# Performance work log

Hardware: AMD Instinct MI355X
Metric: run time of the kernel (lower is better)

## Reference

```python
import jax, jax.numpy as jnp
import numpy as np

T, H, E, K, I = 4096, 1024, 8, 2, 2048
EPS = 1e-5


def setup_inputs() -> dict:
    key = jax.random.key(0)
    ks = jax.random.split(key, 5)
    xavier = jax.nn.initializers.variance_scaling(1.0, 'fan_avg', 'uniform', dtype=jnp.float32)
    return {
        'x': jax.random.normal(ks[0], (T, H), dtype=jnp.float32),
        'scale': jnp.ones((H,), dtype=jnp.float32),
        'gate_kernel': xavier(ks[1], (H, E), jnp.float32),
        'gate_bias': jnp.zeros((E,), dtype=jnp.float32),
        'mlp1_weight': xavier(ks[2], (E, 2 * I, H), jnp.float32),
        'mlp1_bias': jnp.zeros((E, 2 * I), dtype=jnp.float32),
        'mlp2_weight': xavier(ks[3], (E, H, I), jnp.float32),
        'mlp2_bias': jnp.zeros((E, H), dtype=jnp.float32),
    }


def reference(x, scale, gate_kernel, gate_bias, mlp1_weight, mlp1_bias, mlp2_weight, mlp2_bias):
    # RMSNorm in fp32
    t = x.astype(jnp.float32)
    rms = jnp.sqrt(jnp.mean(t * t, axis=-1, keepdims=True) + EPS)
    normed = ((t / rms) * scale).astype(x.dtype)  # [T, H]

    # Gating: top-k experts + softmax over selected logits
    gate_logits = normed @ gate_kernel + gate_bias  # [T, E]
    expert_logits, expert_indices = jax.lax.top_k(gate_logits, K)  # [T, K]
    expert_weights = jax.nn.softmax(expert_logits, axis=-1)  # [T, K]

    # Dense all-expert SwiGLU MLP (faithful to vmap-over-experts original)
    # mlp1_weight: [E, 2I, H] -> mlp1: [E, T, 2I]
    mlp1 = jnp.einsum('td,efd->etf', normed, mlp1_weight) + mlp1_bias[:, None, :]
    gate_part = jnp.minimum(mlp1[..., :I], 7.0)
    linear_part = jnp.clip(mlp1[..., I:], -7.0, 7.0)
    swish_gate = gate_part * jax.nn.sigmoid(1.702 * gate_part)
    activated = swish_gate * (linear_part + 1.0)  # [E, T, I]
    # mlp2_weight: [E, H, I] -> expert_outputs: [T, E, H]
    expert_outputs = (jnp.einsum('eti,ehi->eth', activated, mlp2_weight)
                      + mlp2_bias[:, None, :]).transpose(1, 0, 2)

    # Scatter top-k weights to dense [T, E] and combine
    one_hot = jax.nn.one_hot(expert_indices, E, dtype=expert_outputs.dtype)  # [T, K, E]
    dense_gate_weights = jnp.sum(one_hot * expert_weights[..., None], axis=1)  # [T, E]
    fused = jnp.einsum('teh,te->th', expert_outputs, dense_gate_weights)
    return x + fused
```

## Files before the change

### kernel.cpp

```cpp
#include <hip/hip_runtime.h>
#include <hip/hip_bf16.h>
#include <math.h>

#define T_ 4096
#define H_ 1024
#define E_ 8
#define I_ 2048
#define EPS_ 1e-5f

using bf16x8 = __attribute__((ext_vector_type(8))) short;
using f32x4  = __attribute__((ext_vector_type(4))) float;

static __device__ __forceinline__ unsigned short f2bf(float f) {
    union { float f; unsigned int u; } v; v.f = f;
    unsigned int u = v.u;
    u += 0x7fffu + ((u >> 16) & 1u);
    return (unsigned short)(u >> 16);
}

static __device__ __forceinline__ void gld16(const unsigned short* g, unsigned short* l) {
    __builtin_amdgcn_global_load_lds(
        (const __attribute__((address_space(1))) unsigned int*)g,
        (__attribute__((address_space(3))) unsigned int*)l,
        16, 0, 0);
}

__global__ __launch_bounds__(256) void k_convert(
    const float* __restrict__ src, unsigned short* __restrict__ dst)
{
    size_t i = (size_t)blockIdx.x * 256 + threadIdx.x;
    const float4* s = (const float4*)src + i * 2;
    float4 a = s[0], b = s[1];
    ushort4 lo, hi;
    lo.x = f2bf(a.x); lo.y = f2bf(a.y); lo.z = f2bf(a.z); lo.w = f2bf(a.w);
    hi.x = f2bf(b.x); hi.y = f2bf(b.y); hi.z = f2bf(b.z); hi.w = f2bf(b.w);
    ((ushort4*)dst)[i * 2]     = lo;
    ((ushort4*)dst)[i * 2 + 1] = hi;
}

__global__ __launch_bounds__(256) void k_norm_gate(
    const float* __restrict__ x, const float* __restrict__ scale,
    const float* __restrict__ gk, const float* __restrict__ gb,
    unsigned short* __restrict__ normed_bf,
    int* __restrict__ counts, int* __restrict__ tok_list, float* __restrict__ wtok)
{
    int tid = threadIdx.x;
    int wave = tid >> 6, lane = tid & 63;
    int t = blockIdx.x * 4 + wave;
    const float* xr = x + (size_t)t * H_;
    int h0 = lane * 16;

    float4 xv[4], sv[4];
    #pragma unroll
    for (int c = 0; c < 4; c++) {
        xv[c] = *(const float4*)(xr + h0 + c * 4);
        sv[c] = *(const float4*)(scale + h0 + c * 4);
    }
    float ss = 0.f;
    #pragma unroll
    for (int c = 0; c < 4; c++)
        ss += xv[c].x*xv[c].x + xv[c].y*xv[c].y + xv[c].z*xv[c].z + xv[c].w*xv[c].w;
    #pragma unroll
    for (int off = 32; off; off >>= 1) ss += __shfl_xor(ss, off);
    float inv = 1.0f / sqrtf(ss / (float)H_ + EPS_);

    float nv[16];
    #pragma unroll
    for (int c = 0; c < 4; c++) {
        nv[c*4+0] = xv[c].x * inv * sv[c].x;
        nv[c*4+1] = xv[c].y * inv * sv[c].y;
        nv[c*4+2] = xv[c].z * inv * sv[c].z;
        nv[c*4+3] = xv[c].w * inv * sv[c].w;
    }
    #pragma unroll
    for (int c = 0; c < 4; c++) {
        ushort4 nb;
        nb.x = f2bf(nv[c*4+0]); nb.y = f2bf(nv[c*4+1]);
        nb.z = f2bf(nv[c*4+2]); nb.w = f2bf(nv[c*4+3]);
        *(ushort4*)(normed_bf + (size_t)t * H_ + h0 + c * 4) = nb;
    }

    float p[E_];
    #pragma unroll
    for (int e = 0; e < E_; e++) p[e] = 0.f;
    #pragma unroll
    for (int j = 0; j < 16; j++) {
        const float4* g4 = (const float4*)(gk + (size_t)(h0 + j) * E_);
        float4 a = g4[0], b = g4[1];
        float n = nv[j];
        p[0] += n*a.x; p[1] += n*a.y; p[2] += n*a.z; p[3] += n*a.w;
        p[4] += n*b.x; p[5] += n*b.y; p[6] += n*b.z; p[7] += n*b.w;
    }
    #pragma unroll
    for (int e = 0; e < E_; e++) {
        #pragma unroll
        for (int off = 32; off; off >>= 1) p[e] += __shfl_xor(p[e], off);
    }
    if (lane == 0) {
        int b0 = -1, b1 = -1; float l0 = -1e30f, l1 = -1e30f;
        #pragma unroll
        for (int e = 0; e < E_; e++) {
            float lg = p[e] + gb[e];
            if (lg > l0) { l1 = l0; b1 = b0; l0 = lg; b0 = e; }
            else if (lg > l1) { l1 = lg; b1 = e; }
        }
        float e1 = expf(l1 - l0);
        float w0 = 1.f / (1.f + e1);
        float w1 = e1 / (1.f + e1);
        wtok[t * 2 + 0] = w0;
        wtok[t * 2 + 1] = w1;
        int p0 = atomicAdd(&counts[b0], 1);
        tok_list[b0 * T_ + p0] = t * 2 + 0;
        int p1 = atomicAdd(&counts[b1], 1);
        tok_list[b1 * T_ + p1] = t * 2 + 1;
    }
}

__global__ __launch_bounds__(256) void k_mlp1(
    const unsigned short* __restrict__ w1b,
    const float* __restrict__ b1,
    const unsigned short* __restrict__ normed_bf,
    const int* __restrict__ counts, const int* __restrict__ tok_list,
    unsigned short* __restrict__ act)
{
    int e = blockIdx.z;
    int Ne = counts[e];
    int mt0 = blockIdx.y * 128;
    if (mt0 >= Ne) return;
    int it0 = blockIdx.x * 64;
    int tid = threadIdx.x;
    int lane = tid & 63, w = tid >> 6;
    int quad = lane >> 4, m16 = lane & 15;
    int wr = w >> 1, wc = w & 1;

    __shared__ unsigned short lA[128 * 64];
    __shared__ unsigned short lBg[64 * 64];
    __shared__ unsigned short lBl[64 * 64];
    __shared__ int ls_tk[128];

    if (tid < 128) {
        int slot = mt0 + tid;
        ls_tk[tid] = (slot < Ne) ? tok_list[e * T_ + slot] : -1;
    }

    int lr = lane >> 3;
    int pc = lane & 7;

    const unsigned short* srcA[4];
    #pragma unroll
    for (int it = 0; it < 4; it++) {
        int r = w * 32 + it * 8 + lr;
        int slot = mt0 + r;
        int tk = (slot < Ne) ? tok_list[e * T_ + slot] : 0;
        srcA[it] = normed_bf + (size_t)(tk >> 1) * H_ + ((pc ^ (r & 7)) << 3);
    }
    const size_t w1base = (size_t)e * 2 * I_ * H_;
    const unsigned short* srcG[2];
    const unsigned short* srcL[2];
    #pragma unroll
    for (int it = 0; it < 2; it++) {
        int r = w * 16 + it * 8 + lr;
        srcG[it] = w1b + w1base + (size_t)(it0 + r) * H_ + ((pc ^ (r & 7)) << 3);
        srcL[it] = srcG[it] + (size_t)I_ * H_;
    }

    f32x4 accg[4][2], accl[4][2];
    #pragma unroll
    for (int mi = 0; mi < 4; mi++)
        #pragma unroll
        for (int ni = 0; ni < 2; ni++) {
            accg[mi][ni] = (f32x4){0.f, 0.f, 0.f, 0.f};
            accl[mi][ni] = (f32x4){0.f, 0.f, 0.f, 0.f};
        }

    for (int kk = 0; kk < H_; kk += 64) {
        __syncthreads();
        #pragma unroll
        for (int it = 0; it < 4; it++)
            gld16(srcA[it] + kk, &lA[(w * 32 + it * 8) * 64]);
        #pragma unroll
        for (int it = 0; it < 2; it++) {
            gld16(srcG[it] + kk, &lBg[(w * 16 + it * 8) * 64]);
            gld16(srcL[it] + kk, &lBl[(w * 16 + it * 8) * 64]);
        }
        __syncthreads();
        int m7 = m16 & 7;
        #pragma unroll
        for (int ks = 0; ks < 2; ks++) {
            int jj = ks * 4 + quad;
            bf16x8 af[4], bg[2], bl[2];
            #pragma unroll
            for (int mi = 0; mi < 4; mi++)
                af[mi] = *(const bf16x8*)(&lA[(wr * 64 + mi * 16 + m16) * 64 + ((jj ^ m7) << 3)]);
            #pragma unroll
            for (int ni = 0; ni < 2; ni++) {
                bg[ni] = *(const bf16x8*)(&lBg[(wc * 32 + ni * 16 + m16) * 64 + ((jj ^ m7) << 3)]);
                bl[ni] = *(const bf16x8*)(&lBl[(wc * 32 + ni * 16 + m16) * 64 + ((jj ^ m7) << 3)]);
            }
            #pragma unroll
            for (int mi = 0; mi < 4; mi++)
                #pragma unroll
                for (int ni = 0; ni < 2; ni++) {
                    accg[mi][ni] = __builtin_amdgcn_mfma_f32_16x16x32_bf16(
                        af[mi], bg[ni], accg[mi][ni], 0, 0, 0);
                    accl[mi][ni] = __builtin_amdgcn_mfma_f32_16x16x32_bf16(
                        af[mi], bl[ni], accl[mi][ni], 0, 0, 0);
                }
        }
    }

    const float* b1g = b1 + (size_t)e * 2 * I_;
    const float* b1l = b1g + I_;
    #pragma unroll
    for (int mi = 0; mi < 4; mi++) {
        #pragma unroll
        for (int reg = 0; reg < 4; reg++) {
            int row = wr * 64 + mi * 16 + quad * 4 + reg;
            int tk = ls_tk[row];
            if (tk < 0) continue;
            #pragma unroll
            for (int ni = 0; ni < 2; ni++) {
                int i = it0 + wc * 32 + ni * 16 + m16;
                float g = accg[mi][ni][reg] + b1g[i];
                float l = accl[mi][ni][reg] + b1l[i];
                g = fminf(g, 7.f);
                l = fminf(fmaxf(l, -7.f), 7.f);
                float sw = g / (1.f + expf(-1.702f * g));
                act[(size_t)tk * I_ + i] = f2bf(sw * (l + 1.f));
            }
        }
    }
}

__global__ __launch_bounds__(256) void k_mlp2(
    const unsigned short* __restrict__ w2b,
    const float* __restrict__ b2,
    const unsigned short* __restrict__ act,
    const int* __restrict__ counts, const int* __restrict__ tok_list,
    float* __restrict__ ybuf)
{
    int e = blockIdx.z;
    int Ne = counts[e];
    int mt0 = blockIdx.y * 128;
    if (mt0 >= Ne) return;
    int ht0 = blockIdx.x * 128;
    int tid = threadIdx.x;
    int lane = tid & 63, w = tid >> 6;
    int quad = lane >> 4, m16 = lane & 15;
    int wr = w >> 1, wc = w & 1;

    __shared__ unsigned short lA[128 * 64];
    __shared__ unsigned short lB[128 * 64];
    __shared__ int ls_tk[128];

    if (tid < 128) {
        int slot = mt0 + tid;
        ls_tk[tid] = (slot < Ne) ? tok_list[e * T_ + slot] : -1;
    }

    int lr = lane >> 3;
    int pc = lane & 7;

    const unsigned short* srcA[4];
    #pragma unroll
    for (int it = 0; it < 4; it++) {
        int r = w * 32 + it * 8 + lr;
        int slot = mt0 + r;
        int tk = (slot < Ne) ? tok_list[e * T_ + slot] : 0;
        srcA[it] = act + (size_t)tk * I_ + ((pc ^ (r & 7)) << 3);
    }
    const size_t w2base = (size_t)e * H_ * I_;
    const unsigned short* srcB[4];
    #pragma unroll
    for (int it = 0; it < 4; it++) {
        int r = w * 32 + it * 8 + lr;
        srcB[it] = w2b + w2base + (size_t)(ht0 + r) * I_ + ((pc ^ (r & 7)) << 3);
    }

    f32x4 acc[4][4];
    #pragma unroll
    for (int mi = 0; mi < 4; mi++)
        #pragma unroll
        for (int ni = 0; ni < 4; ni++)
            acc[mi][ni] = (f32x4){0.f, 0.f, 0.f, 0.f};

    for (int kk = 0; kk < I_; kk += 64) {
        __syncthreads();
        #pragma unroll
        for (int it = 0; it < 4; it++)
            gld16(srcA[it] + kk, &lA[(w * 32 + it * 8) * 64]);
        #pragma unroll
        for (int it = 0; it < 4; it++)
            gld16(srcB[it] + kk, &lB[(w * 32 + it * 8) * 64]);
        __syncthreads();
        int m7 = m16 & 7;
        #pragma unroll
        for (int ks = 0; ks < 2; ks++) {
            int jj = ks * 4 + quad;
            bf16x8 af[4], bv[4];
            #pragma unroll
            for (int mi = 0; mi < 4; mi++)
                af[mi] = *(const bf16x8*)(&lA[(wr * 64 + mi * 16 + m16) * 64 + ((jj ^ m7) << 3)]);
            #pragma unroll
            for (int ni = 0; ni < 4; ni++)
                bv[ni] = *(const bf16x8*)(&lB[(wc * 64 + ni * 16 + m16) * 64 + ((jj ^ m7) << 3)]);
            #pragma unroll
            for (int mi = 0; mi < 4; mi++)
                #pragma unroll
                for (int ni = 0; ni < 4; ni++)
                    acc[mi][ni] = __builtin_amdgcn_mfma_f32_16x16x32_bf16(
                        af[mi], bv[ni], acc[mi][ni], 0, 0, 0);
        }
    }

    const float* b2e = b2 + (size_t)e * H_;
    #pragma unroll
    for (int mi = 0; mi < 4; mi++) {
        #pragma unroll
        for (int reg = 0; reg < 4; reg++) {
            int row = wr * 64 + mi * 16 + quad * 4 + reg;
            int tk = ls_tk[row];
            if (tk < 0) continue;
            #pragma unroll
            for (int ni = 0; ni < 4; ni++) {
                int h = ht0 + wc * 64 + ni * 16 + m16;
                ybuf[(size_t)tk * H_ + h] = acc[mi][ni][reg] + b2e[h];
            }
        }
    }
}

__global__ __launch_bounds__(256) void k_combine(
    const float* __restrict__ x, const float* __restrict__ ybuf,
    const float* __restrict__ wtok, float* __restrict__ out)
{
    int t = blockIdx.x;
    int tid = threadIdx.x;
    float w0 = wtok[t * 2 + 0];
    float w1 = wtok[t * 2 + 1];
    float4 xv = ((const float4*)(x + (size_t)t * H_))[tid];
    float4 y0 = ((const float4*)(ybuf + (size_t)(t * 2) * H_))[tid];
    float4 y1 = ((const float4*)(ybuf + (size_t)(t * 2 + 1) * H_))[tid];
    float4 o;
    o.x = xv.x + w0 * y0.x + w1 * y1.x;
    o.y = xv.y + w0 * y0.y + w1 * y1.y;
    o.z = xv.z + w0 * y0.z + w1 * y1.z;
    o.w = xv.w + w0 * y0.w + w1 * y1.w;
    ((float4*)(out + (size_t)t * H_))[tid] = o;
}

extern "C" void kernel_launch(void* const* d_in, const int* in_sizes, int n_in,
                              void* d_out, int out_size, void* d_ws, size_t ws_size,
                              hipStream_t stream) {
    const float* x     = (const float*)d_in[0];
    const float* scale = (const float*)d_in[1];
    const float* gk    = (const float*)d_in[2];
    const float* gb    = (const float*)d_in[3];
    const float* w1    = (const float*)d_in[4];
    const float* b1    = (const float*)d_in[5];
    const float* w2    = (const float*)d_in[6];
    const float* b2    = (const float*)d_in[7];
    float* out = (float*)d_out;

    char* ws = (char*)d_ws;
    const size_t MB = 1024 * 1024;
    unsigned short* normed_bf = (unsigned short*)ws;
    unsigned short* act       = (unsigned short*)(ws + 8 * MB);
    unsigned short* w1b       = (unsigned short*)(ws + 40 * MB);
    float*          ybuf      = (float*)(ws + 40 * MB);
    unsigned short* w2b       = (unsigned short*)(ws + 104 * MB);
    char* ctl                 = ws + 136 * MB;
    int*   counts   = (int*)ctl;
    int*   tok_list = (int*)(ctl + 256);
    float* wtok     = (float*)(ctl + 256 + (size_t)E_ * T_ * 4);

    hipMemsetAsync(counts, 0, E_ * sizeof(int), stream);

    k_norm_gate<<<dim3(T_ / 4), dim3(256), 0, stream>>>(
        x, scale, gk, gb, normed_bf, counts, tok_list, wtok);
    k_convert<<<dim3((E_ * 2 * I_ * H_) / (256 * 8)), dim3(256), 0, stream>>>(w1, w1b);
    k_convert<<<dim3((E_ * H_ * I_) / (256 * 8)), dim3(256), 0, stream>>>(w2, w2b);

    k_mlp1<<<dim3(I_ / 64, T_ / 128, E_), dim3(256), 0, stream>>>(
        w1b, b1, normed_bf, counts, tok_list, act);
    k_mlp2<<<dim3(H_ / 128, T_ / 128, E_), dim3(256), 0, stream>>>(
        w2b, b2, act, counts, tok_list, ybuf);
    k_combine<<<dim3(T_), dim3(256), 0, stream>>>(x, ybuf, wtok, out);
}
```

Measured before the change: 589.8 us.

## Double-buffer LDS tiles in both expert GEMM kernels to overlap loads with MFMA

Both the MLP1 and MLP2 grouped-GEMM kernels now keep two LDS buffers. The global-to-LDS load for the next K slice is issued before the MFMA work on the current slice, and the loop runs two slices per iteration. The aim is to hide global memory latency behind compute and drop one barrier per slice. In exchange, LDS use per block doubles (about 64KB in both kernels), which may lower occupancy. There is also a subtle risk: the asynchronous LDS writes are only ordered by the barriers, so correctness relies on the barrier waiting for outstanding vmcnt.

```diff
diff --git a/kernel.cpp b/kernel.cpp
--- a/kernel.cpp
+++ b/kernel.cpp
@@ -133,9 +133,9 @@
     int quad = lane >> 4, m16 = lane & 15;
     int wr = w >> 1, wc = w & 1;
 
-    __shared__ unsigned short lA[128 * 64];
-    __shared__ unsigned short lBg[64 * 64];
-    __shared__ unsigned short lBl[64 * 64];
+    __shared__ unsigned short lA[2][128 * 64];
+    __shared__ unsigned short lBg[2][64 * 64];
+    __shared__ unsigned short lBl[2][64 * 64];
     __shared__ int ls_tk[128];
 
     if (tid < 128) {
@@ -173,41 +173,58 @@
             accl[mi][ni] = (f32x4){0.f, 0.f, 0.f, 0.f};
         }
 
-    for (int kk = 0; kk < H_; kk += 64) {
+    int m7 = m16 & 7;
+
+#define STAGE1(buf, kk)                                                       \
+    {                                                                          \
+        _Pragma("unroll")                                                      \
+        for (int it = 0; it < 4; it++)                                         \
+            gld16(srcA[it] + (kk), &lA[buf][(w * 32 + it * 8) * 64]);          \
+        _Pragma("unroll")                                                      \
+        for (int it = 0; it < 2; it++) {                                       \
+            gld16(srcG[it] + (kk), &lBg[buf][(w * 16 + it * 8) * 64]);         \
+            gld16(srcL[it] + (kk), &lBl[buf][(w * 16 + it * 8) * 64]);         \
+        }                                                                      \
+    }
+
+#define COMP1(buf)                                                             \
+    {                                                                          \
+        _Pragma("unroll")                                                      \
+        for (int ks = 0; ks < 2; ks++) {                                       \
+            int jj = ks * 4 + quad;                                            \
+            bf16x8 af[4], bg[2], bl[2];                                        \
+            _Pragma("unroll")                                                  \
+            for (int mi = 0; mi < 4; mi++)                                     \
+                af[mi] = *(const bf16x8*)(&lA[buf][(wr * 64 + mi * 16 + m16) * 64 + ((jj ^ m7) << 3)]); \
+            _Pragma("unroll")                                                  \
+            for (int ni = 0; ni < 2; ni++) {                                   \
+                bg[ni] = *(const bf16x8*)(&lBg[buf][(wc * 32 + ni * 16 + m16) * 64 + ((jj ^ m7) << 3)]); \
+                bl[ni] = *(const bf16x8*)(&lBl[buf][(wc * 32 + ni * 16 + m16) * 64 + ((jj ^ m7) << 3)]); \
+            }                                                                  \
+            _Pragma("unroll")                                                  \
+            for (int mi = 0; mi < 4; mi++)                                     \
+                _Pragma("unroll")                                              \
+                for (int ni = 0; ni < 2; ni++) {                               \
+                    accg[mi][ni] = __builtin_amdgcn_mfma_f32_16x16x32_bf16(    \
+                        af[mi], bg[ni], accg[mi][ni], 0, 0, 0);                \
+                    accl[mi][ni] = __builtin_amdgcn_mfma_f32_16x16x32_bf16(    \
+                        af[mi], bl[ni], accl[mi][ni], 0, 0, 0);                \
+                }                                                              \
+        }                                                                      \
+    }
+
+    STAGE1(0, 0);
+    __syncthreads();
+    for (int kk = 0; kk < H_; kk += 128) {
+        STAGE1(1, kk + 64);
+        COMP1(0);
         __syncthreads();
-        #pragma unroll
-        for (int it = 0; it < 4; it++)
-            gld16(srcA[it] + kk, &lA[(w * 32 + it * 8) * 64]);
-        #pragma unroll
-        for (int it = 0; it < 2; it++) {
-            gld16(srcG[it] + kk, &lBg[(w * 16 + it * 8) * 64]);
-            gld16(srcL[it] + kk, &lBl[(w * 16 + it * 8) * 64]);
-        }
+        if (kk + 128 < H_) STAGE1(0, kk + 128);
+        COMP1(1);
         __syncthreads();
-        int m7 = m16 & 7;
-        #pragma unroll
-        for (int ks = 0; ks < 2; ks++) {
-            int jj = ks * 4 + quad;
-            bf16x8 af[4], bg[2], bl[2];
-            #pragma unroll
-            for (int mi = 0; mi < 4; mi++)
-                af[mi] = *(const bf16x8*)(&lA[(wr * 64 + mi * 16 + m16) * 64 + ((jj ^ m7) << 3)]);
-            #pragma unroll
-            for (int ni = 0; ni < 2; ni++) {
-                bg[ni] = *(const bf16x8*)(&lBg[(wc * 32 + ni * 16 + m16) * 64 + ((jj ^ m7) << 3)]);
-                bl[ni] = *(const bf16x8*)(&lBl[(wc * 32 + ni * 16 + m16) * 64 + ((jj ^ m7) << 3)]);
-            }
-            #pragma unroll
-            for (int mi = 0; mi < 4; mi++)
-                #pragma unroll
-                for (int ni = 0; ni < 2; ni++) {
-                    accg[mi][ni] = __builtin_amdgcn_mfma_f32_16x16x32_bf16(
-                        af[mi], bg[ni], accg[mi][ni], 0, 0, 0);
-                    accl[mi][ni] = __builtin_amdgcn_mfma_f32_16x16x32_bf16(
-                        af[mi], bl[ni], accl[mi][ni], 0, 0, 0);
-                }
-        }
-    }
+    }
+#undef STAGE1
+#undef COMP1
 
     const float* b1g = b1 + (size_t)e * 2 * I_;
     const float* b1l = b1g + I_;
@@ -249,8 +266,8 @@
     int quad = lane >> 4, m16 = lane & 15;
     int wr = w >> 1, wc = w & 1;
 
-    __shared__ unsigned short lA[128 * 64];
-    __shared__ unsigned short lB[128 * 64];
+    __shared__ unsigned short lA[2][128 * 64];
+    __shared__ unsigned short lB[2][128 * 64];
     __shared__ int ls_tk[128];
 
     if (tid < 128) {
@@ -284,34 +301,51 @@
         for (int ni = 0; ni < 4; ni++)
             acc[mi][ni] = (f32x4){0.f, 0.f, 0.f, 0.f};
 
-    for (int kk = 0; kk < I_; kk += 64) {
+    int m7 = m16 & 7;
+
+#define STAGE2(buf, kk)                                                       \
+    {                                                                          \
+        _Pragma("unroll")                                                      \
+        for (int it = 0; it < 4; it++)                                         \
+            gld16(srcA[it] + (kk), &lA[buf][(w * 32 + it * 8) * 64]);          \
+        _Pragma("unroll")                                                      \
+        for (int it = 0; it < 4; it++)                                         \
+            gld16(srcB[it] + (kk), &lB[buf][(w * 32 + it * 8) * 64]);          \
+    }
+
+#define COMP2(buf)                                                             \
+    {                                                                          \
+        _Pragma("unroll")                                                      \
+        for (int ks = 0; ks < 2; ks++) {                                       \
+            int jj = ks * 4 + quad;                                            \
+            bf16x8 af[4], bv[4];                                               \
+            _Pragma("unroll")                                                  \
+            for (int mi = 0; mi < 4; mi++)                                     \
+                af[mi] = *(const bf16x8*)(&lA[buf][(wr * 64 + mi * 16 + m16) * 64 + ((jj ^ m7) << 3)]); \
+            _Pragma("unroll")                                                  \
+            for (int ni = 0; ni < 4; ni++)                                     \
+                bv[ni] = *(const bf16x8*)(&lB[buf][(wc * 64 + ni * 16 + m16) * 64 + ((jj ^ m7) << 3)]); \
+            _Pragma("unroll")                                                  \
+            for (int mi = 0; mi < 4; mi++)                                     \
+                _Pragma("unroll")                                              \
+                for (int ni = 0; ni < 4; ni++)                                 \
+                    acc[mi][ni] = __builtin_amdgcn_mfma_f32_16x16x32_bf16(     \
+                        af[mi], bv[ni], acc[mi][ni], 0, 0, 0);                 \
+        }                                                                      \
+    }
+
+    STAGE2(0, 0);
+    __syncthreads();
+    for (int kk = 0; kk < I_; kk += 128) {
+        STAGE2(1, kk + 64);
+        COMP2(0);
         __syncthreads();
-        #pragma unroll
-        for (int it = 0; it < 4; it++)
-            gld16(srcA[it] + kk, &lA[(w * 32 + it * 8) * 64]);
-        #pragma unroll
-        for (int it = 0; it < 4; it++)
-            gld16(srcB[it] + kk, &lB[(w * 32 + it * 8) * 64]);
+        if (kk + 128 < I_) STAGE2(0, kk + 128);
+        COMP2(1);
         __syncthreads();
-        int m7 = m16 & 7;
-        #pragma unroll
-        for (int ks = 0; ks < 2; ks++) {
-            int jj = ks * 4 + quad;
-            bf16x8 af[4], bv[4];
-            #pragma unroll
-            for (int mi = 0; mi < 4; mi++)
-                af[mi] = *(const bf16x8*)(&lA[(wr * 64 + mi * 16 + m16) * 64 + ((jj ^ m7) << 3)]);
-            #pragma unroll
-            for (int ni = 0; ni < 4; ni++)
-                bv[ni] = *(const bf16x8*)(&lB[(wc * 64 + ni * 16 + m16) * 64 + ((jj ^ m7) << 3)]);
-            #pragma unroll
-            for (int mi = 0; mi < 4; mi++)
-                #pragma unroll
-                for (int ni = 0; ni < 4; ni++)
-                    acc[mi][ni] = __builtin_amdgcn_mfma_f32_16x16x32_bf16(
-                        af[mi], bv[ni], acc[mi][ni], 0, 0, 0);
-        }
-    }
+    }
+#undef STAGE2
+#undef COMP2
 
     const float* b2e = b2 + (size_t)e * H_;
     #pragma unroll
```

After: 609.1 us. 3.3% more time.

## Register-prefetch GEMM tiles, retile mlp1, and merge weight conversion kernels

Applied to the files above, without the earlier changes.

Both expert GEMM kernels stop using direct global-to-LDS loads. They now prefetch the next K-slice into registers while computing the current one, then write it into swizzled LDS, so global latency overlaps with MFMA work. mlp1 is retiled from 128 tokens by 64 I-columns to 64 tokens by 128 I-columns, which reuses each token row across more weight columns. The two fp32-to-bf16 weight conversions are merged into one launch. In exchange the kernels use more registers and write to LDS through VGPRs, and the smaller token tile reads the mlp1 weights more often.

```diff
diff --git a/kernel.cpp b/kernel.cpp
--- a/kernel.cpp
+++ b/kernel.cpp
@@ -18,17 +18,17 @@
     return (unsigned short)(u >> 16);
 }
 
-static __device__ __forceinline__ void gld16(const unsigned short* g, unsigned short* l) {
-    __builtin_amdgcn_global_load_lds(
-        (const __attribute__((address_space(1))) unsigned int*)g,
-        (__attribute__((address_space(3))) unsigned int*)l,
-        16, 0, 0);
-}
-
-__global__ __launch_bounds__(256) void k_convert(
-    const float* __restrict__ src, unsigned short* __restrict__ dst)
-{
-    size_t i = (size_t)blockIdx.x * 256 + threadIdx.x;
+__global__ __launch_bounds__(256) void k_convert2(
+    const float* __restrict__ s1, unsigned short* __restrict__ d1,
+    const float* __restrict__ s2, unsigned short* __restrict__ d2,
+    int nb1)
+{
+    int bx = blockIdx.x;
+    const float* src;
+    unsigned short* dst;
+    size_t i;
+    if (bx < nb1) { src = s1; dst = d1; i = (size_t)bx * 256 + threadIdx.x; }
+    else          { src = s2; dst = d2; i = (size_t)(bx - nb1) * 256 + threadIdx.x; }
     const float4* s = (const float4*)src + i * 2;
     float4 a = s[0], b = s[1];
     ushort4 lo, hi;
@@ -125,82 +125,87 @@
 {
     int e = blockIdx.z;
     int Ne = counts[e];
-    int mt0 = blockIdx.y * 128;
+    int mt0 = blockIdx.y * 64;
     if (mt0 >= Ne) return;
-    int it0 = blockIdx.x * 64;
+    int it0 = blockIdx.x * 128;
     int tid = threadIdx.x;
     int lane = tid & 63, w = tid >> 6;
     int quad = lane >> 4, m16 = lane & 15;
     int wr = w >> 1, wc = w & 1;
-
-    __shared__ unsigned short lA[128 * 64];
-    __shared__ unsigned short lBg[64 * 64];
-    __shared__ unsigned short lBl[64 * 64];
-    __shared__ int ls_tk[128];
-
-    if (tid < 128) {
-        int slot = mt0 + tid;
-        ls_tk[tid] = (slot < Ne) ? tok_list[e * T_ + slot] : -1;
-    }
-
-    int lr = lane >> 3;
-    int pc = lane & 7;
-
-    const unsigned short* srcA[4];
-    #pragma unroll
-    for (int it = 0; it < 4; it++) {
-        int r = w * 32 + it * 8 + lr;
-        int slot = mt0 + r;
-        int tk = (slot < Ne) ? tok_list[e * T_ + slot] : 0;
-        srcA[it] = normed_bf + (size_t)(tk >> 1) * H_ + ((pc ^ (r & 7)) << 3);
-    }
-    const size_t w1base = (size_t)e * 2 * I_ * H_;
-    const unsigned short* srcG[2];
-    const unsigned short* srcL[2];
-    #pragma unroll
-    for (int it = 0; it < 2; it++) {
-        int r = w * 16 + it * 8 + lr;
-        srcG[it] = w1b + w1base + (size_t)(it0 + r) * H_ + ((pc ^ (r & 7)) << 3);
-        srcL[it] = srcG[it] + (size_t)I_ * H_;
-    }
-
-    f32x4 accg[4][2], accl[4][2];
-    #pragma unroll
-    for (int mi = 0; mi < 4; mi++)
-        #pragma unroll
-        for (int ni = 0; ni < 2; ni++) {
+    int m7 = m16 & 7;
+
+    __shared__ unsigned short lA[64 * 64];
+    __shared__ unsigned short lBg[128 * 64];
+    __shared__ unsigned short lBl[128 * 64];
+
+    f32x4 accg[2][4], accl[2][4];
+    #pragma unroll
+    for (int mi = 0; mi < 2; mi++)
+        #pragma unroll
+        for (int ni = 0; ni < 4; ni++) {
             accg[mi][ni] = (f32x4){0.f, 0.f, 0.f, 0.f};
             accl[mi][ni] = (f32x4){0.f, 0.f, 0.f, 0.f};
         }
 
+    const size_t w1base = (size_t)e * 2 * I_ * H_;
+    int rA = tid >> 3, sgA = tid & 7;
+    int jA = sgA ^ (rA & 7);
+    int rB = tid >> 1, sgB = tid & 1;
+
+    int slot0 = mt0 + rA, slot1 = mt0 + rA + 32;
+    int tk0 = (slot0 < Ne) ? tok_list[e * T_ + slot0] : -1;
+    int tk1 = (slot1 < Ne) ? tok_list[e * T_ + slot1] : -1;
+    const unsigned short* sA0 = normed_bf + (size_t)((tk0 < 0) ? 0 : (tk0 >> 1)) * H_ + sgA * 8;
+    const unsigned short* sA1 = normed_bf + (size_t)((tk1 < 0) ? 0 : (tk1 >> 1)) * H_ + sgA * 8;
+    const unsigned short* sG = w1b + w1base + (size_t)(it0 + rB) * H_ + sgB * 32;
+    const unsigned short* sL = sG + (size_t)I_ * H_;
+
+    uint4 ra0, ra1, rg[4], rl[4];
+    ra0 = *(const uint4*)(sA0);
+    ra1 = *(const uint4*)(sA1);
+    #pragma unroll
+    for (int q = 0; q < 4; q++) {
+        rg[q] = ((const uint4*)sG)[q];
+        rl[q] = ((const uint4*)sL)[q];
+    }
+
     for (int kk = 0; kk < H_; kk += 64) {
         __syncthreads();
-        #pragma unroll
-        for (int it = 0; it < 4; it++)
-            gld16(srcA[it] + kk, &lA[(w * 32 + it * 8) * 64]);
-        #pragma unroll
-        for (int it = 0; it < 2; it++) {
-            gld16(srcG[it] + kk, &lBg[(w * 16 + it * 8) * 64]);
-            gld16(srcL[it] + kk, &lBl[(w * 16 + it * 8) * 64]);
+        *(uint4*)(&lA[rA * 64 + jA * 8])        = ra0;
+        *(uint4*)(&lA[(rA + 32) * 64 + jA * 8]) = ra1;
+        #pragma unroll
+        for (int q = 0; q < 4; q++) {
+            int jc = (4 * sgB + q) ^ (rB & 7);
+            *(uint4*)(&lBg[rB * 64 + jc * 8]) = rg[q];
+            *(uint4*)(&lBl[rB * 64 + jc * 8]) = rl[q];
         }
         __syncthreads();
-        int m7 = m16 & 7;
-        #pragma unroll
-        for (int ks = 0; ks < 2; ks++) {
-            int jj = ks * 4 + quad;
-            bf16x8 af[4], bg[2], bl[2];
-            #pragma unroll
-            for (int mi = 0; mi < 4; mi++)
-                af[mi] = *(const bf16x8*)(&lA[(wr * 64 + mi * 16 + m16) * 64 + ((jj ^ m7) << 3)]);
-            #pragma unroll
-            for (int ni = 0; ni < 2; ni++) {
-                bg[ni] = *(const bf16x8*)(&lBg[(wc * 32 + ni * 16 + m16) * 64 + ((jj ^ m7) << 3)]);
-                bl[ni] = *(const bf16x8*)(&lBl[(wc * 32 + ni * 16 + m16) * 64 + ((jj ^ m7) << 3)]);
-            }
-            #pragma unroll
-            for (int mi = 0; mi < 4; mi++)
+        if (kk + 64 < H_) {
+            int k2 = kk + 64;
+            ra0 = *(const uint4*)(sA0 + k2);
+            ra1 = *(const uint4*)(sA1 + k2);
+            #pragma unroll
+            for (int q = 0; q < 4; q++) {
+                rg[q] = ((const uint4*)(sG + k2))[q];
+                rl[q] = ((const uint4*)(sL + k2))[q];
+            }
+        }
+        #pragma unroll
+        for (int ks2 = 0; ks2 < 2; ks2++) {
+            int jj = ks2 * 4 + quad;
+            bf16x8 af[2], bg[4], bl[4];
+            #pragma unroll
+            for (int mi = 0; mi < 2; mi++)
+                af[mi] = *(const bf16x8*)(&lA[(wr * 32 + mi * 16 + m16) * 64 + ((jj ^ m7) << 3)]);
+            #pragma unroll
+            for (int ni = 0; ni < 4; ni++) {
+                bg[ni] = *(const bf16x8*)(&lBg[(wc * 64 + ni * 16 + m16) * 64 + ((jj ^ m7) << 3)]);
+                bl[ni] = *(const bf16x8*)(&lBl[(wc * 64 + ni * 16 + m16) * 64 + ((jj ^ m7) << 3)]);
+            }
+            #pragma unroll
+            for (int mi = 0; mi < 2; mi++)
                 #pragma unroll
-                for (int ni = 0; ni < 2; ni++) {
+                for (int ni = 0; ni < 4; ni++) {
                     accg[mi][ni] = __builtin_amdgcn_mfma_f32_16x16x32_bf16(
                         af[mi], bg[ni], accg[mi][ni], 0, 0, 0);
                     accl[mi][ni] = __builtin_amdgcn_mfma_f32_16x16x32_bf16(
@@ -212,15 +217,16 @@
     const float* b1g = b1 + (size_t)e * 2 * I_;
     const float* b1l = b1g + I_;
     #pragma unroll
-    for (int mi = 0; mi < 4; mi++) {
+    for (int mi = 0; mi < 2; mi++) {
         #pragma unroll
         for (int reg = 0; reg < 4; reg++) {
-            int row = wr * 64 + mi * 16 + quad * 4 + reg;
-            int tk = ls_tk[row];
-            if (tk < 0) continue;
-            #pragma unroll
-            for (int ni = 0; ni < 2; ni++) {
-                int i = it0 + wc * 32 + ni * 16 + m16;
+            int row = wr * 32 + mi * 16 + quad * 4 + reg;
+            int slot = mt0 + row;
+            if (slot >= Ne) continue;
+            int tk = tok_list[e * T_ + slot];
+            #pragma unroll
+            for (int ni = 0; ni < 4; ni++) {
+                int i = it0 + wc * 64 + ni * 16 + m16;
                 float g = accg[mi][ni][reg] + b1g[i];
                 float l = accl[mi][ni][reg] + b1l[i];
                 g = fminf(g, 7.f);
@@ -248,34 +254,10 @@
     int lane = tid & 63, w = tid >> 6;
     int quad = lane >> 4, m16 = lane & 15;
     int wr = w >> 1, wc = w & 1;
+    int m7 = m16 & 7;
 
     __shared__ unsigned short lA[128 * 64];
     __shared__ unsigned short lB[128 * 64];
-    __shared__ int ls_tk[128];
-
-    if (tid < 128) {
-        int slot = mt0 + tid;
-        ls_tk[tid] = (slot < Ne) ? tok_list[e * T_ + slot] : -1;
-    }
-
-    int lr = lane >> 3;
-    int pc = lane & 7;
-
-    const unsigned short* srcA[4];
-    #pragma unroll
-    for (int it = 0; it < 4; it++) {
-        int r = w * 32 + it * 8 + lr;
-        int slot = mt0 + r;
-        int tk = (slot < Ne) ? tok_list[e * T_ + slot] : 0;
-        srcA[it] = act + (size_t)tk * I_ + ((pc ^ (r & 7)) << 3);
-    }
-    const size_t w2base = (size_t)e * H_ * I_;
-    const unsigned short* srcB[4];
-    #pragma unroll
-    for (int it = 0; it < 4; it++) {
-        int r = w * 32 + it * 8 + lr;
-        srcB[it] = w2b + w2base + (size_t)(ht0 + r) * I_ + ((pc ^ (r & 7)) << 3);
-    }
 
     f32x4 acc[4][4];
     #pragma unroll
@@ -284,19 +266,41 @@
         for (int ni = 0; ni < 4; ni++)
             acc[mi][ni] = (f32x4){0.f, 0.f, 0.f, 0.f};
 
+    const size_t w2base = (size_t)e * H_ * I_;
+    int rA = tid >> 1, sgA = tid & 1;
+
+    int slotA = mt0 + rA;
+    int tkA = (slotA < Ne) ? tok_list[e * T_ + slotA] : -1;
+    const unsigned short* sA = act + (size_t)((tkA < 0) ? 0 : tkA) * I_ + sgA * 32;
+    const unsigned short* sB = w2b + w2base + (size_t)(ht0 + rA) * I_ + sgA * 32;
+
+    uint4 ra[4], rb[4];
+    #pragma unroll
+    for (int q = 0; q < 4; q++) {
+        ra[q] = ((const uint4*)sA)[q];
+        rb[q] = ((const uint4*)sB)[q];
+    }
+
     for (int kk = 0; kk < I_; kk += 64) {
         __syncthreads();
         #pragma unroll
-        for (int it = 0; it < 4; it++)
-            gld16(srcA[it] + kk, &lA[(w * 32 + it * 8) * 64]);
-        #pragma unroll
-        for (int it = 0; it < 4; it++)
-            gld16(srcB[it] + kk, &lB[(w * 32 + it * 8) * 64]);
+        for (int q = 0; q < 4; q++) {
+            int jc = (4 * sgA + q) ^ (rA & 7);
+            *(uint4*)(&lA[rA * 64 + jc * 8]) = ra[q];
+            *(uint4*)(&lB[rA * 64 + jc * 8]) = rb[q];
+        }
         __syncthreads();
-        int m7 = m16 & 7;
-        #pragma unroll
-        for (int ks = 0; ks < 2; ks++) {
-            int jj = ks * 4 + quad;
+        if (kk + 64 < I_) {
+            int k2 = kk + 64;
+            #pragma unroll
+            for (int q = 0; q < 4; q++) {
+                ra[q] = ((const uint4*)(sA + k2))[q];
+                rb[q] = ((const uint4*)(sB + k2))[q];
+            }
+        }
+        #pragma unroll
+        for (int ks2 = 0; ks2 < 2; ks2++) {
+            int jj = ks2 * 4 + quad;
             bf16x8 af[4], bv[4];
             #pragma unroll
             for (int mi = 0; mi < 4; mi++)
@@ -319,8 +323,9 @@
         #pragma unroll
         for (int reg = 0; reg < 4; reg++) {
             int row = wr * 64 + mi * 16 + quad * 4 + reg;
-            int tk = ls_tk[row];
-            if (tk < 0) continue;
+            int slot = mt0 + row;
+            if (slot >= Ne) continue;
+            int tk = tok_list[e * T_ + slot];
             #pragma unroll
             for (int ni = 0; ni < 4; ni++) {
                 int h = ht0 + wc * 64 + ni * 16 + m16;
@@ -378,10 +383,12 @@
 
     k_norm_gate<<<dim3(T_ / 4), dim3(256), 0, stream>>>(
         x, scale, gk, gb, normed_bf, counts, tok_list, wtok);
-    k_convert<<<dim3((E_ * 2 * I_ * H_) / (256 * 8)), dim3(256), 0, stream>>>(w1, w1b);
-    k_convert<<<dim3((E_ * H_ * I_) / (256 * 8)), dim3(256), 0, stream>>>(w2, w2b);
-
-    k_mlp1<<<dim3(I_ / 64, T_ / 128, E_), dim3(256), 0, stream>>>(
+
+    int nb1 = (E_ * 2 * I_ * H_) / (256 * 8);
+    int nb2 = (E_ * H_ * I_) / (256 * 8);
+    k_convert2<<<dim3(nb1 + nb2), dim3(256), 0, stream>>>(w1, w1b, w2, w2b, nb1);
+
+    k_mlp1<<<dim3(I_ / 128, T_ / 64, E_), dim3(256), 0, stream>>>(
         w1b, b1, normed_bf, counts, tok_list, act);
     k_mlp2<<<dim3(H_ / 128, T_ / 128, E_), dim3(256), 0, stream>>>(
         w2b, b2, act, counts, tok_list, ybuf);
```

After: 1.070 ms. 1.81x slower.
